# Kernel optimization log

Measured on AMD Instinct MI355X. Metric: run time of the kernel, lower is better.

The kernel has to match this reference:

```python
import jax, jax.numpy as jnp
import numpy as np

H_FWD, H_REV, M = 25, 25, 3        # n=3, m=3 hardcoded in module
IN_SIZE = 4 * H_REV + 1            # 101 = H_rev + (n-2) + H_rev*m
UNITS = 512
BATCH = 8192
INPUT_SIZE = H_REV + (3 - 2) + (H_FWD + H_REV) * M  # 176


def setup_inputs() -> dict:
    key = jax.random.key(0)
    ks = jax.random.split(key, 6)
    x = jax.random.normal(ks[0], (BATCH, INPUT_SIZE), jnp.float32)

    def lin(k, fi, fo):
        kw, kb = jax.random.split(k)
        W = jax.random.normal(kw, (fi, fo), jnp.float32) / np.float32(np.sqrt(fi))
        b = jax.random.normal(kb, (fo,), jnp.float32) * 0.01
        return W, b

    W0, b0 = lin(ks[1], IN_SIZE, UNITS)
    W1, b1 = lin(ks[2], UNITS, UNITS)
    W2, b2 = lin(ks[3], UNITS, UNITS)
    W3, b3 = lin(ks[4], UNITS, UNITS)
    W4, b4 = lin(ks[5], UNITS, 1)
    return dict(x=x, W0=W0, b0=b0, W1=W1, b1=b1, W2=W2, b2=b2,
                W3=W3, b3=b3, W4=W4, b4=b4)


def _mlp(params, d):
    # Tanh MLP, final Linear to scalar; returns (B,)
    h = d
    for W, b in params[:-1]:
        h = jnp.tanh(h @ W + b)
    W, b = params[-1]
    return (h @ W + b)[:, 0]


def reference(x, W0, b0, W1, b1, W2, b2, W3, b3, W4, b4):
    params = [(W0, b0), (W1, b1), (W2, b2), (W3, b3), (W4, b4)]
    B = x.shape[0]
    e = x[:, :H_REV]                                   # (B, H_rev)
    v = x[:, -(H_FWD + H_REV) * M:].reshape(B, H_FWD + H_REV, M)
    f = lambda d: _mlp(params, d)

    w_cols, grads = [], []
    for i in range(H_FWD):  # strictly sequential recursion over horizon
        if i < H_REV:
            if i > 0:
                w_seg = jax.lax.stop_gradient(jnp.stack(w_cols, axis=1))
            else:
                w_seg = jnp.zeros((B, 0), x.dtype)
            data = jnp.concatenate(
                [e[:, i:], w_seg,
                 v[:, i:i + H_REV].reshape(B, -1),
                 jnp.full((B, 1), float(i), x.dtype)], axis=1)
        else:
            w_seg = jax.lax.stop_gradient(jnp.stack(w_cols[i - H_REV:i], axis=1))
            data = jnp.concatenate(
                [w_seg, v[:, i:i + H_REV].reshape(B, -1),
                 jnp.full((B, 1), float(i), x.dtype)], axis=1)
        out, vjp_fn = jax.vjp(f, data)      # out: (B,), scalar output per sample
        g, = vjp_fn(jnp.ones_like(out))     # (B, IN_SIZE): per-step Jacobian row
        w_cols.append(out)
        grads.append(g)

    w = jnp.stack(w_cols, axis=1)           # (B, H_fwd)
    grad = jnp.stack(grads, axis=1)         # (B, H_fwd, IN_SIZE)
    return w, grad
```

## Files before the change

kernel.cpp:

```cpp
#include <hip/hip_runtime.h>

#define B_ROWS 8192
#define UNITS 512
#define NITER 25
#define INSZ 176
#define KPAD 128
#define GRAD_COLS 101

typedef __attribute__((ext_vector_type(8))) short short8;
typedef __attribute__((ext_vector_type(4))) float f32x4;
typedef __attribute__((ext_vector_type(8))) _Float16 half8;

__device__ __forceinline__ unsigned short f2h_bits(float f) {
  _Float16 h = (_Float16)f;
  return __builtin_bit_cast(unsigned short, h);
}
__device__ __forceinline__ float h2f_bits(unsigned short b) {
  return (float)__builtin_bit_cast(_Float16, b);
}
__device__ __forceinline__ float fast_tanh(float x) {
  float e = __expf(2.0f * x);
  return 1.0f - 2.0f / (e + 1.0f);
}

typedef __attribute__((address_space(3))) unsigned int lds_u32;
typedef __attribute__((address_space(1))) const unsigned int glb_u32;
__device__ __forceinline__ void gload16(const void* g, void* l) {
  __builtin_amdgcn_global_load_lds((glb_u32*)g, (lds_u32*)l, 16, 0, 0);
}

__device__ __forceinline__ f32x4 mf(short8 a, short8 b, f32x4 c) {
  return __builtin_amdgcn_mfma_f32_16x16x32_f16(
      __builtin_bit_cast(half8, a), __builtin_bit_cast(half8, b), c, 0, 0, 0);
}

struct GArgs {
  const unsigned short *A;
  const unsigned short *B;
  int K;
  const float* bias;
  const unsigned short *Hh;
  unsigned short *Oh;
  float* Og;
  int iter;
  const float* W4p;
};

__global__ __launch_bounds__(256)
void prep_kernel(const float* __restrict__ W0, const float* __restrict__ W1,
                 const float* __restrict__ W2, const float* __restrict__ W3,
                 unsigned short* TW0, unsigned short* TW1,
                 unsigned short* TW2, unsigned short* TW3,
                 unsigned short* CW0, unsigned short* CW1,
                 unsigned short* CW2, unsigned short* CW3,
                 float* w_acc)
{
  int id = blockIdx.x * 256 + threadIdx.x;
  if (id < NITER * B_ROWS) w_acc[id] = 0.0f;
  if (id < 512 * KPAD) {
    int n = id >> 7, k = id & (KPAD - 1);
    TW0[id] = f2h_bits((k < 101) ? W0[(size_t)k * 512 + n] : 0.0f);
    int n2 = id >> 9, k2 = id & 511;
    CW0[id] = f2h_bits((n2 < 101) ? W0[(size_t)n2 * 512 + k2] : 0.0f);
  }
  {
    int n = id >> 9, k = id & 511;
    TW1[id] = f2h_bits(W1[(size_t)k * 512 + n]);
    TW2[id] = f2h_bits(W2[(size_t)k * 512 + n]);
    TW3[id] = f2h_bits(W3[(size_t)k * 512 + n]);
    CW1[id] = f2h_bits(W1[id]);
    CW2[id] = f2h_bits(W2[id]);
    CW3[id] = f2h_bits(W3[id]);
  }
}

__global__ __launch_bounds__(256)
void build_d0_kernel(const float* __restrict__ x, unsigned short* __restrict__ D)
{
  int id = blockIdx.x * 256 + threadIdx.x;
  int b = id >> 7, c = id & 127;
  float val;
  if (c < 25)             val = x[(size_t)b * INSZ + c];
  else if (c < 100)       val = x[(size_t)b * INSZ + 26 + (c - 25)];
  else                    val = 0.0f;
  D[id] = f2h_bits(val);
}

template<int EPI>
__global__ __launch_bounds__(256, 2)
void fwd_kernel(GArgs g)
{
  __shared__ short smem[24576];
  const int t = threadIdx.x;
  const int w = t >> 6;
  const int lane = t & 63;
  const int l15 = lane & 15, l4 = lane >> 4;
  const int id = blockIdx.x;
  const int bm = (id & 7) | ((id >> 5) << 3);
  const int bn = (id >> 3) & 3;
  const int wm = (w >> 1) * 32, wn = (w & 1) * 64;
  const int K = g.K;
  const int NK = K >> 6;
  f32x4 acc[2][4] = {};

  const int sr = t >> 3;
  const int ss = t & 7;

  auto stage = [&](int ks, int buf) {
    short* As = smem + buf * 12288;
    short* Bs = As + 4096;
    int kc = ks << 6;
#pragma unroll
    for (int q = 0; q < 2; ++q) {
      int r = q * 32 + sr;
      int c = ss ^ (r & 7);
      size_t ga = (size_t)(bm * 64 + r) * K + kc + c * 8;
      gload16(g.A + ga, &As[q * 2048 + w * 512]);
    }
#pragma unroll
    for (int q = 0; q < 4; ++q) {
      int r = q * 32 + sr;
      int c = ss ^ (r & 7);
      size_t gb = (size_t)(bn * 128 + r) * K + kc + c * 8;
      gload16(g.B + gb, &Bs[q * 2048 + w * 512]);
    }
  };

  stage(0, 0);
  for (int ks = 0; ks < NK; ++ks) {
    if (ks + 1 < NK) {
      stage(ks + 1, (ks + 1) & 1);
      asm volatile("s_waitcnt vmcnt(6)" ::: "memory");
    } else {
      asm volatile("s_waitcnt vmcnt(0)" ::: "memory");
    }
    __builtin_amdgcn_sched_barrier(0);
    __builtin_amdgcn_s_barrier();

    const short* As = smem + (ks & 1) * 12288;
    const short* Bs = As + 4096;
#pragma unroll
    for (int kk = 0; kk < 2; ++kk) {
      short8 av[2], bh[4];
#pragma unroll
      for (int mi = 0; mi < 2; ++mi) {
        int row = wm + mi * 16 + l15;
        av[mi] = *(const short8*)&As[row * 64 + (((kk * 4 + l4) ^ (row & 7)) << 3)];
      }
#pragma unroll
      for (int ni = 0; ni < 4; ++ni) {
        int row = wn + ni * 16 + l15;
        bh[ni] = *(const short8*)&Bs[row * 64 + (((kk * 4 + l4) ^ (row & 7)) << 3)];
      }
#pragma unroll
      for (int mi = 0; mi < 2; ++mi)
#pragma unroll
        for (int ni = 0; ni < 4; ++ni)
          acc[mi][ni] = mf(av[mi], bh[ni], acc[mi][ni]);
    }
    asm volatile("s_waitcnt lgkmcnt(0)" ::: "memory");
    __builtin_amdgcn_sched_barrier(0);
    __builtin_amdgcn_s_barrier();
  }

  const int gm0 = bm * 64 + wm;
  const int gn0 = bn * 128 + wn;
  float wp[2][4] = {};
#pragma unroll
  for (int mi = 0; mi < 2; ++mi) {
#pragma unroll
    for (int ni = 0; ni < 4; ++ni) {
      int n = gn0 + ni * 16 + l15;
#pragma unroll
      for (int r = 0; r < 4; ++r) {
        int m = gm0 + mi * 16 + l4 * 4 + r;
        float v = acc[mi][ni][r];
        float h = fast_tanh(v + g.bias[n]);
        if constexpr (EPI == 0) {
          g.Oh[(size_t)m * UNITS + n] = f2h_bits(h);
        } else {
          float w4 = g.W4p[n];
          g.Oh[(size_t)m * UNITS + n] = f2h_bits((1.0f - h * h) * w4);
          wp[mi][r] += h * w4;
        }
      }
    }
  }
  if constexpr (EPI == 3) {
#pragma unroll
    for (int mi = 0; mi < 2; ++mi)
#pragma unroll
      for (int r = 0; r < 4; ++r) {
        float v = wp[mi][r];
        v += __shfl_xor(v, 1); v += __shfl_xor(v, 2);
        v += __shfl_xor(v, 4); v += __shfl_xor(v, 8);
        if (l15 == 0) {
          int m = gm0 + mi * 16 + l4 * 4 + r;
          atomicAdd(&g.Og[m], v);
        }
      }
  }
}

template<int EPI>
__global__ __launch_bounds__(256, 2)
void bwd_kernel(GArgs g)
{
  __shared__ short smem[32768];
  const int t = threadIdx.x;
  const int w = t >> 6;
  const int lane = t & 63;
  const int l15 = lane & 15, l4 = lane >> 4;
  const int id = blockIdx.x;
  const int bm = (EPI == 2) ? id : ((id & 7) | ((id >> 5) << 3));
  const int bn = (EPI == 2) ? 0  : ((id >> 3) & 3);
  const int wm = (w >> 1) * 64, wn = (w & 1) * 64;
  const int K = g.K;
  const int NK = K >> 6;
  f32x4 acc[4][4] = {};

  const int sr = t >> 3;
  const int ss = t & 7;

  auto stage = [&](int ks, int buf) {
    short* As = smem + buf * 16384;
    short* Bs = As + 8192;
    int kc = ks << 6;
#pragma unroll
    for (int q = 0; q < 4; ++q) {
      int r = q * 32 + sr;
      int c = ss ^ (r & 7);
      size_t ga = (size_t)(bm * 128 + r) * K + kc + c * 8;
      size_t gb = (size_t)(bn * 128 + r) * K + kc + c * 8;
      int ldst = q * 2048 + w * 512;
      gload16(g.A + ga, &As[ldst]);
      gload16(g.B + gb, &Bs[ldst]);
    }
  };

  stage(0, 0);
  for (int ks = 0; ks < NK; ++ks) {
    if (ks + 1 < NK) {
      stage(ks + 1, (ks + 1) & 1);
      asm volatile("s_waitcnt vmcnt(8)" ::: "memory");
    } else {
      asm volatile("s_waitcnt vmcnt(0)" ::: "memory");
    }
    __builtin_amdgcn_sched_barrier(0);
    __builtin_amdgcn_s_barrier();

    const short* As = smem + (ks & 1) * 16384;
    const short* Bs = As + 8192;
#pragma unroll
    for (int kk = 0; kk < 2; ++kk) {
      short8 av[4], bh[4];
#pragma unroll
      for (int mi = 0; mi < 4; ++mi) {
        int row = wm + mi * 16 + l15;
        av[mi] = *(const short8*)&As[row * 64 + (((kk * 4 + l4) ^ (row & 7)) << 3)];
      }
#pragma unroll
      for (int ni = 0; ni < 4; ++ni) {
        int row = wn + ni * 16 + l15;
        bh[ni] = *(const short8*)&Bs[row * 64 + (((kk * 4 + l4) ^ (row & 7)) << 3)];
      }
#pragma unroll
      for (int mi = 0; mi < 4; ++mi)
#pragma unroll
        for (int ni = 0; ni < 4; ++ni)
          acc[mi][ni] = mf(av[mi], bh[ni], acc[mi][ni]);
    }
    asm volatile("s_waitcnt lgkmcnt(0)" ::: "memory");
    __builtin_amdgcn_sched_barrier(0);
    __builtin_amdgcn_s_barrier();
  }

  const int gm0 = bm * 128 + wm;
  const int gn0 = bn * 128 + wn;
#pragma unroll
  for (int mi = 0; mi < 4; ++mi) {
#pragma unroll
    for (int ni = 0; ni < 4; ++ni) {
      int n = gn0 + ni * 16 + l15;
#pragma unroll
      for (int r = 0; r < 4; ++r) {
        int m = gm0 + mi * 16 + l4 * 4 + r;
        float v = acc[mi][ni][r];
        if constexpr (EPI == 1) {
          size_t idx = (size_t)m * UNITS + n;
          float h = h2f_bits(g.Hh[idx]);
          g.Oh[idx] = f2h_bits(v * (1.0f - h * h));
        } else {
          if (n < GRAD_COLS) {
            int it = m >> 13, b = m & 8191;
            g.Og[((size_t)b * NITER + (g.iter + it)) * GRAD_COLS + n] = v;
          }
        }
      }
    }
  }
}

__global__ __launch_bounds__(256)
void build_dw_kernel(const float* __restrict__ x, const float* __restrict__ w_acc,
                     const float* __restrict__ b4, float* __restrict__ w_out,
                     unsigned short* __restrict__ D, int iter)
{
  int id = blockIdx.x * 256 + threadIdx.x;
  int b = id >> 7, c = id & 127;
  float wv = w_acc[(size_t)iter * B_ROWS + b] + b4[0];
  if (c == 0) w_out[(size_t)b * NITER + iter] = wv;
  if (iter < NITER - 1) {
    int jn = iter + 1;
    float val;
    if (c < 25 - jn)        val = x[(size_t)b * INSZ + jn + c];
    else if (c < 24)        val = w_out[(size_t)b * NITER + (c - (25 - jn))];
    else if (c == 24)       val = wv;
    else if (c < 100)       val = x[(size_t)b * INSZ + 26 + 3 * jn + (c - 25)];
    else if (c == 100)      val = (float)jn;
    else                    val = 0.0f;
    D[(size_t)b * KPAD + c] = f2h_bits(val);
  }
}

extern "C" void kernel_launch(void* const* d_in, const int* in_sizes, int n_in,
                              void* d_out, int out_size, void* d_ws, size_t ws_size,
                              hipStream_t stream) {
  const float* x  = (const float*)d_in[0];
  const float* W0 = (const float*)d_in[1];
  const float* b0 = (const float*)d_in[2];
  const float* W1 = (const float*)d_in[3];
  const float* b1 = (const float*)d_in[4];
  const float* W2 = (const float*)d_in[5];
  const float* b2 = (const float*)d_in[6];
  const float* W3 = (const float*)d_in[7];
  const float* b3 = (const float*)d_in[8];
  const float* W4 = (const float*)d_in[9];
  const float* b4 = (const float*)d_in[10];

  float* w_out    = (float*)d_out;
  float* grad_out = (float*)d_out + (size_t)B_ROWS * NITER;

  const size_t SL    = (size_t)B_ROWS * UNITS;
  const size_t FIXED = 3407872 + 2097152 + 819200 + 4096;
  int CH = 1;
  {
    const int lad[4] = {25, 5, 3, 2};
    for (int k = 0; k < 4; ++k) {
      size_t need = FIXED + (size_t)lad[k] * 5 * SL * 2;
      if (ws_size >= need) { CH = lad[k]; break; }
    }
  }

  char* p = (char*)d_ws;
  auto alloc = [&](size_t elems) { unsigned short* r = (unsigned short*)p; p += elems * 2; return r; };

  unsigned short* TW0 = alloc(512 * KPAD);
  unsigned short* TW1 = alloc(512 * 512);
  unsigned short* TW2 = alloc(512 * 512);
  unsigned short* TW3 = alloc(512 * 512);
  unsigned short* CW0 = alloc(KPAD * 512);
  unsigned short* CW1 = alloc(512 * 512);
  unsigned short* CW2 = alloc(512 * 512);
  unsigned short* CW3 = alloc(512 * 512);
  unsigned short* D   = alloc((size_t)B_ROWS * KPAD);
  float* w_acc = (float*)p; p += (size_t)NITER * B_ROWS * 4;

  unsigned short* H0w = alloc((size_t)CH * SL);
  unsigned short* H1w = alloc((size_t)CH * SL);
  unsigned short* H2w = alloc((size_t)CH * SL);
  unsigned short* U3w = alloc((size_t)CH * SL);
  unsigned short* Ubw = alloc((size_t)CH * SL);

  prep_kernel<<<1024, 256, 0, stream>>>(W0, W1, W2, W3,
      TW0, TW1, TW2, TW3, CW0, CW1, CW2, CW3, w_acc);
  build_d0_kernel<<<4096, 256, 0, stream>>>(x, D);

  for (int j0 = 0; j0 < NITER; j0 += CH) {
    int wlen = (NITER - j0 < CH) ? (NITER - j0) : CH;
    for (int it = 0; it < wlen; ++it) {
      int i = j0 + it;
      unsigned short* H0s = H0w + (size_t)it * SL;
      unsigned short* H1s = H1w + (size_t)it * SL;
      unsigned short* H2s = H2w + (size_t)it * SL;
      unsigned short* U3s = U3w + (size_t)it * SL;
      GArgs f0 = {D,   TW0, KPAD, b0, nullptr, H0s, nullptr, 0, nullptr};
      GArgs f1 = {H0s, TW1, 512,  b1, nullptr, H1s, nullptr, 0, nullptr};
      GArgs f2 = {H1s, TW2, 512,  b2, nullptr, H2s, nullptr, 0, nullptr};
      GArgs f3 = {H2s, TW3, 512,  b3, nullptr, U3s, w_acc + (size_t)i * B_ROWS, 0, W4};
      fwd_kernel<0><<<512, 256, 0, stream>>>(f0);
      fwd_kernel<0><<<512, 256, 0, stream>>>(f1);
      fwd_kernel<0><<<512, 256, 0, stream>>>(f2);
      fwd_kernel<3><<<512, 256, 0, stream>>>(f3);
      build_dw_kernel<<<4096, 256, 0, stream>>>(x, w_acc, b4, w_out, D, i);
    }
    GArgs bw3 = {U3w, CW3, 512, nullptr, H2w, Ubw, nullptr, 0, nullptr};
    GArgs bw2 = {Ubw, CW2, 512, nullptr, H1w, U3w, nullptr, 0, nullptr};
    GArgs bw1 = {U3w, CW1, 512, nullptr, H0w, Ubw, nullptr, 0, nullptr};
    GArgs gr0 = {Ubw, CW0, 512, nullptr, nullptr, nullptr, grad_out, j0, nullptr};
    bwd_kernel<1><<<wlen * 256, 256, 0, stream>>>(bw3);
    bwd_kernel<1><<<wlen * 256, 256, 0, stream>>>(bw2);
    bwd_kernel<1><<<wlen * 256, 256, 0, stream>>>(bw1);
    bwd_kernel<2><<<wlen * 64,  256, 0, stream>>>(gr0);
  }

  (void)in_sizes; (void)n_in; (void)out_size;
}
```

Measured before the change: 2.001 ms.

## Pair backward GEMMs of step i with forward GEMMs of step i+1 in one launch

Replaces the chunked schedule (all forwards first, then batched backward over CH iterations) with a software-pipelined schedule. Each launch runs one backward layer of iteration i alongside one forward layer of iteration i+1, using double-buffered activation storage. The backward GEMM now uses the 64x128 tile path with 3 blocks per CU instead of the larger 128x128 tile. The aim is to fill the GPU with more concurrent blocks per launch and cut launch count, at the cost of smaller backward tiles and no longer batching backward work across iterations.

```diff
diff --git a/kernel.cpp b/kernel.cpp
--- a/kernel.cpp
+++ b/kernel.cpp
@@ -87,17 +87,14 @@
 }
 
 template<int EPI>
-__global__ __launch_bounds__(256, 2)
-void fwd_kernel(GArgs g)
+__device__ __forceinline__ void gemm64(const GArgs g, short* smem, int id)
 {
-  __shared__ short smem[24576];
   const int t = threadIdx.x;
   const int w = t >> 6;
   const int lane = t & 63;
   const int l15 = lane & 15, l4 = lane >> 4;
-  const int id = blockIdx.x;
-  const int bm = (id & 7) | ((id >> 5) << 3);
-  const int bn = (id >> 3) & 3;
+  const int bm = (EPI == 2) ? id : ((id & 7) | ((id >> 5) << 3));
+  const int bn = (EPI == 2) ? 0  : ((id >> 3) & 3);
   const int wm = (w >> 1) * 32, wn = (w & 1) * 64;
   const int K = g.K;
   const int NK = K >> 6;
@@ -175,10 +172,18 @@
       for (int r = 0; r < 4; ++r) {
         int m = gm0 + mi * 16 + l4 * 4 + r;
         float v = acc[mi][ni][r];
-        float h = fast_tanh(v + g.bias[n]);
         if constexpr (EPI == 0) {
+          float h = fast_tanh(v + g.bias[n]);
           g.Oh[(size_t)m * UNITS + n] = f2h_bits(h);
+        } else if constexpr (EPI == 1) {
+          size_t idx = (size_t)m * UNITS + n;
+          float h = h2f_bits(g.Hh[idx]);
+          g.Oh[idx] = f2h_bits(v * (1.0f - h * h));
+        } else if constexpr (EPI == 2) {
+          if (n < GRAD_COLS)
+            g.Og[((size_t)m * NITER + g.iter) * GRAD_COLS + n] = v;
         } else {
+          float h = fast_tanh(v + g.bias[n]);
           float w4 = g.W4p[n];
           g.Oh[(size_t)m * UNITS + n] = f2h_bits((1.0f - h * h) * w4);
           wp[mi][r] += h * w4;
@@ -202,103 +207,20 @@
   }
 }
 
-template<int EPI>
-__global__ __launch_bounds__(256, 2)
-void bwd_kernel(GArgs g)
-{
-  __shared__ short smem[32768];
-  const int t = threadIdx.x;
-  const int w = t >> 6;
-  const int lane = t & 63;
-  const int l15 = lane & 15, l4 = lane >> 4;
-  const int id = blockIdx.x;
-  const int bm = (EPI == 2) ? id : ((id & 7) | ((id >> 5) << 3));
-  const int bn = (EPI == 2) ? 0  : ((id >> 3) & 3);
-  const int wm = (w >> 1) * 64, wn = (w & 1) * 64;
-  const int K = g.K;
-  const int NK = K >> 6;
-  f32x4 acc[4][4] = {};
-
-  const int sr = t >> 3;
-  const int ss = t & 7;
-
-  auto stage = [&](int ks, int buf) {
-    short* As = smem + buf * 16384;
-    short* Bs = As + 8192;
-    int kc = ks << 6;
-#pragma unroll
-    for (int q = 0; q < 4; ++q) {
-      int r = q * 32 + sr;
-      int c = ss ^ (r & 7);
-      size_t ga = (size_t)(bm * 128 + r) * K + kc + c * 8;
-      size_t gb = (size_t)(bn * 128 + r) * K + kc + c * 8;
-      int ldst = q * 2048 + w * 512;
-      gload16(g.A + ga, &As[ldst]);
-      gload16(g.B + gb, &Bs[ldst]);
-    }
-  };
-
-  stage(0, 0);
-  for (int ks = 0; ks < NK; ++ks) {
-    if (ks + 1 < NK) {
-      stage(ks + 1, (ks + 1) & 1);
-      asm volatile("s_waitcnt vmcnt(8)" ::: "memory");
-    } else {
-      asm volatile("s_waitcnt vmcnt(0)" ::: "memory");
-    }
-    __builtin_amdgcn_sched_barrier(0);
-    __builtin_amdgcn_s_barrier();
-
-    const short* As = smem + (ks & 1) * 16384;
-    const short* Bs = As + 8192;
-#pragma unroll
-    for (int kk = 0; kk < 2; ++kk) {
-      short8 av[4], bh[4];
-#pragma unroll
-      for (int mi = 0; mi < 4; ++mi) {
-        int row = wm + mi * 16 + l15;
-        av[mi] = *(const short8*)&As[row * 64 + (((kk * 4 + l4) ^ (row & 7)) << 3)];
-      }
-#pragma unroll
-      for (int ni = 0; ni < 4; ++ni) {
-        int row = wn + ni * 16 + l15;
-        bh[ni] = *(const short8*)&Bs[row * 64 + (((kk * 4 + l4) ^ (row & 7)) << 3)];
-      }
-#pragma unroll
-      for (int mi = 0; mi < 4; ++mi)
-#pragma unroll
-        for (int ni = 0; ni < 4; ++ni)
-          acc[mi][ni] = mf(av[mi], bh[ni], acc[mi][ni]);
-    }
-    asm volatile("s_waitcnt lgkmcnt(0)" ::: "memory");
-    __builtin_amdgcn_sched_barrier(0);
-    __builtin_amdgcn_s_barrier();
-  }
-
-  const int gm0 = bm * 128 + wm;
-  const int gn0 = bn * 128 + wn;
-#pragma unroll
-  for (int mi = 0; mi < 4; ++mi) {
-#pragma unroll
-    for (int ni = 0; ni < 4; ++ni) {
-      int n = gn0 + ni * 16 + l15;
-#pragma unroll
-      for (int r = 0; r < 4; ++r) {
-        int m = gm0 + mi * 16 + l4 * 4 + r;
-        float v = acc[mi][ni][r];
-        if constexpr (EPI == 1) {
-          size_t idx = (size_t)m * UNITS + n;
-          float h = h2f_bits(g.Hh[idx]);
-          g.Oh[idx] = f2h_bits(v * (1.0f - h * h));
-        } else {
-          if (n < GRAD_COLS) {
-            int it = m >> 13, b = m & 8191;
-            g.Og[((size_t)b * NITER + (g.iter + it)) * GRAD_COLS + n] = v;
-          }
-        }
-      }
-    }
-  }
+template<int EA, int EB>
+__global__ __launch_bounds__(256, 3)
+void paired_kernel(GArgs A, GArgs B, int nA) {
+  __shared__ short smem[24576];
+  int id = blockIdx.x;
+  if (id < nA) gemm64<EA>(A, smem, id);
+  else         gemm64<EB>(B, smem, id - nA);
+}
+
+template<int E>
+__global__ __launch_bounds__(256, 3)
+void solo_kernel(GArgs A) {
+  __shared__ short smem[24576];
+  gemm64<E>(A, smem, blockIdx.x);
 }
 
 __global__ __launch_bounds__(256)
@@ -341,17 +263,6 @@
   float* w_out    = (float*)d_out;
   float* grad_out = (float*)d_out + (size_t)B_ROWS * NITER;
 
-  const size_t SL    = (size_t)B_ROWS * UNITS;
-  const size_t FIXED = 3407872 + 2097152 + 819200 + 4096;
-  int CH = 1;
-  {
-    const int lad[4] = {25, 5, 3, 2};
-    for (int k = 0; k < 4; ++k) {
-      size_t need = FIXED + (size_t)lad[k] * 5 * SL * 2;
-      if (ws_size >= need) { CH = lad[k]; break; }
-    }
-  }
-
   char* p = (char*)d_ws;
   auto alloc = [&](size_t elems) { unsigned short* r = (unsigned short*)p; p += elems * 2; return r; };
 
@@ -366,43 +277,58 @@
   unsigned short* D   = alloc((size_t)B_ROWS * KPAD);
   float* w_acc = (float*)p; p += (size_t)NITER * B_ROWS * 4;
 
-  unsigned short* H0w = alloc((size_t)CH * SL);
-  unsigned short* H1w = alloc((size_t)CH * SL);
-  unsigned short* H2w = alloc((size_t)CH * SL);
-  unsigned short* U3w = alloc((size_t)CH * SL);
-  unsigned short* Ubw = alloc((size_t)CH * SL);
+  const size_t SL = (size_t)B_ROWS * UNITS;
+  unsigned short *H0[2], *H1[2], *H2[2], *U3[2];
+  for (int par = 0; par < 2; ++par) {
+    H0[par] = alloc(SL); H1[par] = alloc(SL);
+    H2[par] = alloc(SL); U3[par] = alloc(SL);
+  }
+  unsigned short* Ub = alloc(SL);
+  unsigned short* Uc = alloc(SL);
 
   prep_kernel<<<1024, 256, 0, stream>>>(W0, W1, W2, W3,
       TW0, TW1, TW2, TW3, CW0, CW1, CW2, CW3, w_acc);
   build_d0_kernel<<<4096, 256, 0, stream>>>(x, D);
 
-  for (int j0 = 0; j0 < NITER; j0 += CH) {
-    int wlen = (NITER - j0 < CH) ? (NITER - j0) : CH;
-    for (int it = 0; it < wlen; ++it) {
-      int i = j0 + it;
-      unsigned short* H0s = H0w + (size_t)it * SL;
-      unsigned short* H1s = H1w + (size_t)it * SL;
-      unsigned short* H2s = H2w + (size_t)it * SL;
-      unsigned short* U3s = U3w + (size_t)it * SL;
-      GArgs f0 = {D,   TW0, KPAD, b0, nullptr, H0s, nullptr, 0, nullptr};
-      GArgs f1 = {H0s, TW1, 512,  b1, nullptr, H1s, nullptr, 0, nullptr};
-      GArgs f2 = {H1s, TW2, 512,  b2, nullptr, H2s, nullptr, 0, nullptr};
-      GArgs f3 = {H2s, TW3, 512,  b3, nullptr, U3s, w_acc + (size_t)i * B_ROWS, 0, W4};
-      fwd_kernel<0><<<512, 256, 0, stream>>>(f0);
-      fwd_kernel<0><<<512, 256, 0, stream>>>(f1);
-      fwd_kernel<0><<<512, 256, 0, stream>>>(f2);
-      fwd_kernel<3><<<512, 256, 0, stream>>>(f3);
-      build_dw_kernel<<<4096, 256, 0, stream>>>(x, w_acc, b4, w_out, D, i);
-    }
-    GArgs bw3 = {U3w, CW3, 512, nullptr, H2w, Ubw, nullptr, 0, nullptr};
-    GArgs bw2 = {Ubw, CW2, 512, nullptr, H1w, U3w, nullptr, 0, nullptr};
-    GArgs bw1 = {U3w, CW1, 512, nullptr, H0w, Ubw, nullptr, 0, nullptr};
-    GArgs gr0 = {Ubw, CW0, 512, nullptr, nullptr, nullptr, grad_out, j0, nullptr};
-    bwd_kernel<1><<<wlen * 256, 256, 0, stream>>>(bw3);
-    bwd_kernel<1><<<wlen * 256, 256, 0, stream>>>(bw2);
-    bwd_kernel<1><<<wlen * 256, 256, 0, stream>>>(bw1);
-    bwd_kernel<2><<<wlen * 64,  256, 0, stream>>>(gr0);
-  }
-
-  (void)in_sizes; (void)n_in; (void)out_size;
-}
+  {
+    GArgs f0 = {D, TW0, KPAD, b0, nullptr, H0[0], nullptr, 0, nullptr};
+    GArgs f1 = {H0[0], TW1, 512, b1, nullptr, H1[0], nullptr, 0, nullptr};
+    GArgs f2 = {H1[0], TW2, 512, b2, nullptr, H2[0], nullptr, 0, nullptr};
+    GArgs f3 = {H2[0], TW3, 512, b3, nullptr, U3[0], w_acc, 0, W4};
+    solo_kernel<0><<<512, 256, 0, stream>>>(f0);
+    solo_kernel<0><<<512, 256, 0, stream>>>(f1);
+    solo_kernel<0><<<512, 256, 0, stream>>>(f2);
+    solo_kernel<3><<<512, 256, 0, stream>>>(f3);
+  }
+
+  for (int i = 0; i < NITER; ++i) {
+    int pp = i & 1, q = pp ^ 1;
+    bool more = (i < NITER - 1);
+
+    build_dw_kernel<<<4096, 256, 0, stream>>>(x, w_acc, b4, w_out, D, i);
+
+    GArgs bw3 = {U3[pp], CW3, 512, nullptr, H2[pp], Ub, nullptr, 0, nullptr};
+    GArgs bw2 = {Ub,     CW2, 512, nullptr, H1[pp], Uc, nullptr, 0, nullptr};
+    GArgs bw1 = {Uc,     CW1, 512, nullptr, H0[pp], Ub, nullptr, 0, nullptr};
+    GArgs gr0 = {Ub,     CW0, 512, nullptr, nullptr, nullptr, grad_out, i, nullptr};
+
+    if (more) {
+      GArgs f0 = {D, TW0, KPAD, b0, nullptr, H0[q], nullptr, 0, nullptr};
+      GArgs f1 = {H0[q], TW1, 512, b1, nullptr, H1[q], nullptr, 0, nullptr};
+      GArgs f2 = {H1[q], TW2, 512, b2, nullptr, H2[q], nullptr, 0, nullptr};
+      GArgs f3 = {H2[q], TW3, 512, b3, nullptr, U3[q],
+                  w_acc + (size_t)(i + 1) * B_ROWS, 0, W4};
+      paired_kernel<1, 0><<<1024, 256, 0, stream>>>(bw3, f0, 512);
+      paired_kernel<1, 0><<<1024, 256, 0, stream>>>(bw2, f1, 512);
+      paired_kernel<1, 0><<<1024, 256, 0, stream>>>(bw1, f2, 512);
+      paired_kernel<2, 3><<<640,  256, 0, stream>>>(gr0, f3, 128);
+    } else {
+      solo_kernel<1><<<512, 256, 0, stream>>>(bw3);
+      solo_kernel<1><<<512, 256, 0, stream>>>(bw2);
+      solo_kernel<1><<<512, 256, 0, stream>>>(bw1);
+      solo_kernel<2><<<128, 256, 0, stream>>>(gr0);
+    }
+  }
+
+  (void)in_sizes; (void)n_in; (void)out_size; (void)ws_size;
+}
```

After: 1.728 ms. 1.16x faster.
